# Performance work log

Measured on AMD Instinct MI355X. Metric: run time of the kernel, lower is better.

Reference implementation:

```python
import jax, jax.numpy as jnp
import numpy as np

B, L, H, M, V = 8, 1024, 1024, 128, 32
LN_EPS = 1e-5


def setup_inputs() -> dict:
    key = jax.random.key(0)
    ks = jax.random.split(key, 6)
    x_enc = jax.random.normal(ks[0], (B, L, H), dtype=jnp.float32)
    ln_gamma = jnp.ones((H,), jnp.float32)
    ln_beta = jnp.zeros((H,), jnp.float32)
    Wq = jax.random.normal(ks[1], (H, H), jnp.float32) * 0.02
    Wk = jax.random.normal(ks[2], (H, H), jnp.float32) * 0.02
    W_embed = jax.random.normal(ks[3], (V * V, H), jnp.float32) * 0.02
    W_mlm = jax.random.normal(ks[4], (V, H), jnp.float32) * 0.02
    # masked positions per sequence: contiguous span [1, M] (token 0 at pos 0,
    # token 2 at pos M+1 in the original encoding); sorted, in-range, static M.
    mask_idx = jnp.tile(jnp.arange(1, M + 1, dtype=jnp.int32)[None, :], (B, 1))
    return {"x_enc": x_enc, "ln_gamma": ln_gamma, "ln_beta": ln_beta,
            "Wq": Wq, "Wk": Wk, "W_embed": W_embed, "W_mlm": W_mlm,
            "mask_idx": mask_idx}


def _layer_norm(x, gamma, beta):
    mu = jnp.mean(x, axis=-1, keepdims=True)
    var = jnp.mean(jnp.square(x - mu), axis=-1, keepdims=True)
    return (x - mu) * jax.lax.rsqrt(var + LN_EPS) * gamma + beta


def reference(x_enc, ln_gamma, ln_beta, Wq, Wk, W_embed, W_mlm, mask_idx):
    x = _layer_norm(x_enc, ln_gamma, ln_beta)            # [B,L,H]
    mlm_logits = jnp.einsum('blh,vh->blv', x, W_mlm)      # [B,L,V]

    # ragged masked-span gather (static M masked positions per sequence)
    masked_x = jnp.take_along_axis(x, mask_idx[:, :, None].astype(jnp.int32), axis=1)  # [B,M,H]
    q = jnp.einsum('bmh,oh->bmo', masked_x, Wq)           # fc_pmlm_q, no bias
    k = jnp.einsum('bmh,oh->bmo', masked_x, Wk)           # fc_pmlm_k, no bias
    pairs = jnp.einsum('bih,bjh->bijh', q, k)             # per-span outer product [B,M,M,H]
    pairs = pairs.reshape(B * M * M, H)
    logits = jnp.einsum('nh,vh->nv', pairs, W_embed)      # [B*M*M, V*V]

    diag_mask = jnp.tile(jnp.eye(M, dtype=bool).reshape(-1), B)  # [B*M*M]

    in_span = jnp.zeros((B, L), jnp.int8).at[jnp.arange(B)[:, None], mask_idx].set(1)
    mask_aa = in_span[:, :, None]                                      # [B,L,1]
    pair_mask_aa = (in_span[:, :, None] * in_span[:, None, :])[..., None]  # [B,L,L,1] int8

    return logits, mlm_logits, diag_mask, mask_aa, pair_mask_aa
```

## Files before the change

kernel.cpp:

```cpp
#include <hip/hip_runtime.h>


typedef float   f32x4 __attribute__((ext_vector_type(4)));
typedef _Float16 f16x8 __attribute__((ext_vector_type(8)));

__device__ __forceinline__ void gld16(const void* g, void* l) {
  __builtin_amdgcn_global_load_lds(
      (const __attribute__((address_space(1))) void*)g,
      (__attribute__((address_space(3))) void*)l, 16, 0, 0);
}

__global__ __launch_bounds__(256) void cvt_kernel(
    const float* __restrict__ wq, const float* __restrict__ wk,
    const float* __restrict__ we, const float* __restrict__ wm,
    _Float16* __restrict__ oq, _Float16* __restrict__ ok,
    _Float16* __restrict__ oe, _Float16* __restrict__ om) {
  int id = blockIdx.x * 256 + threadIdx.x;
  const float* src; _Float16* dst; int off;
  if (id < 262144)      { src = wq; dst = oq; off = id; }
  else if (id < 524288) { src = wk; dst = ok; off = id - 262144; }
  else if (id < 786432) { src = we; dst = oe; off = id - 524288; }
  else                  { src = wm; dst = om; off = id - 786432; }
  float4 v = ((const float4*)src)[off];
  union { _Float16 h[4]; uint2 u; } o;
  o.h[0] = (_Float16)v.x; o.h[1] = (_Float16)v.y;
  o.h[2] = (_Float16)v.z; o.h[3] = (_Float16)v.w;
  ((uint2*)dst)[off] = o.u;
}

__global__ __launch_bounds__(256) void ln_kernel(
    const float* __restrict__ x, const float* __restrict__ g,
    const float* __restrict__ be, _Float16* __restrict__ xo) {
  const int row = blockIdx.x, t = threadIdx.x;
  const float4 v = ((const float4*)(x + (size_t)row * 1024))[t];
  float s1 = v.x + v.y + v.z + v.w;
  float s2 = v.x * v.x + v.y * v.y + v.z * v.z + v.w * v.w;
  #pragma unroll
  for (int m = 1; m < 64; m <<= 1) {
    s1 += __shfl_xor(s1, m, 64);
    s2 += __shfl_xor(s2, m, 64);
  }
  __shared__ float red[8];
  const int w = t >> 6, lane = t & 63;
  if (lane == 0) { red[w * 2] = s1; red[w * 2 + 1] = s2; }
  __syncthreads();
  s1 = red[0] + red[2] + red[4] + red[6];
  s2 = red[1] + red[3] + red[5] + red[7];
  const float mu = s1 * (1.f / 1024.f);
  const float var = s2 * (1.f / 1024.f) - mu * mu;
  const float rs = rsqrtf(var + 1e-5f);
  const float4 gv = ((const float4*)g)[t];
  const float4 bv = ((const float4*)be)[t];
  union { _Float16 h[4]; uint2 u; } o;
  o.h[0] = (_Float16)((v.x - mu) * rs * gv.x + bv.x);
  o.h[1] = (_Float16)((v.y - mu) * rs * gv.y + bv.y);
  o.h[2] = (_Float16)((v.z - mu) * rs * gv.z + bv.z);
  o.h[3] = (_Float16)((v.w - mu) * rs * gv.w + bv.w);
  ((uint2*)(xo + (size_t)row * 1024))[t] = o.u;
}

__global__ __launch_bounds__(256, 4) void qk_gemm(
    const _Float16* __restrict__ xh, const _Float16* __restrict__ wq,
    const _Float16* __restrict__ wk, const int* __restrict__ midx,
    _Float16* __restrict__ qout, _Float16* __restrict__ kout) {
  __shared__ _Float16 at[64 * 32];
  __shared__ _Float16 bt[64 * 32];
  const int tid = threadIdx.x, w = tid >> 6, lane = tid & 63;
  const int l15 = lane & 15, quad = lane >> 4;
  const int ntile = blockIdx.x, rtile = blockIdx.y, mat = blockIdx.z;
  const _Float16* wmat = mat ? wk : wq;
  _Float16* outp = mat ? kout : qout;

  const int arow = tid >> 2;
  const int acol = (tid & 3) * 8;
  const int grow = rtile * 64 + arow;
  const int b = grow >> 7, m = grow & 127;
  const int src = midx[b * 128 + m];
  const _Float16* agp = xh + ((size_t)(b * 1024 + src)) * 1024 + acol;
  const _Float16* bgp = wmat + (size_t)(ntile * 64 + arow) * 1024 + acol;
  char* aldst = (char*)at + w * 1024;
  char* bldst = (char*)bt + w * 1024;

  f32x4 acc[4];
  const f32x4 zero = {0.f, 0.f, 0.f, 0.f};
  #pragma unroll
  for (int ns = 0; ns < 4; ++ns) acc[ns] = zero;

  for (int s = 0; s < 32; ++s) {
    const int kk = s * 32;
    gld16(agp + kk, aldst);
    gld16(bgp + kk, bldst);
    __syncthreads();
    const f16x8 af = *(const f16x8*)&at[(w * 16 + l15) * 32 + quad * 8];
    #pragma unroll
    for (int ns = 0; ns < 4; ++ns) {
      const f16x8 bf = *(const f16x8*)&bt[(ns * 16 + l15) * 32 + quad * 8];
      acc[ns] = __builtin_amdgcn_mfma_f32_16x16x32_f16(af, bf, acc[ns], 0, 0, 0);
    }
    __syncthreads();
  }
  #pragma unroll
  for (int ns = 0; ns < 4; ++ns) {
    const int col = ntile * 64 + ns * 16 + l15;
    #pragma unroll
    for (int r = 0; r < 4; ++r) {
      const int row = rtile * 64 + w * 16 + quad * 4 + r;
      outp[(size_t)row * 1024 + col] = (_Float16)acc[ns][r];
    }
  }
}

__global__ __launch_bounds__(256, 3) void big_gemm(
    const _Float16* __restrict__ qf, const _Float16* __restrict__ kf,
    const _Float16* __restrict__ wemb, float* __restrict__ out) {
  __shared__ _Float16 kt[128 * 32];
  __shared__ _Float16 btile[128 * 32];
  __shared__ _Float16 qrow[1024];

  const int tid = threadIdx.x, w = tid >> 6, lane = tid & 63;
  const int l15 = lane & 15, quad = lane >> 4;
  const int vtile = blockIdx.x;
  const int rt = blockIdx.y;
  const int b = rt >> 7, i = rt & 127;
  const int wm = w >> 1, wn = w & 1;

  const _Float16* kbase = kf + (size_t)b * 128 * 1024;
  const _Float16* qbase = qf + (size_t)(b * 128 + i) * 1024;
  const _Float16* wbase = wemb + (size_t)vtile * 128 * 1024;

  if (w < 2) gld16(qbase + w * 512 + lane * 8, (char*)qrow + w * 1024);

  f32x4 acc[4][4];
  const f32x4 zero = {0.f, 0.f, 0.f, 0.f};
  #pragma unroll
  for (int a = 0; a < 4; ++a)
    #pragma unroll
    for (int c = 0; c < 4; ++c) acc[a][c] = zero;

  const int srow0 = w * 32 + (lane >> 2);
  const int scol = (lane & 3) * 8;

  for (int s = 0; s < 32; ++s) {
    const int kk = s * 32;
    #pragma unroll
    for (int p = 0; p < 2; ++p) {
      const int r = srow0 + p * 16;
      gld16(kbase + (size_t)r * 1024 + kk + scol,
            (char*)kt + w * 2048 + p * 1024);
      gld16(wbase + (size_t)r * 1024 + kk + scol,
            (char*)btile + w * 2048 + p * 1024);
    }
    __syncthreads();

    const f16x8 qs = *(const f16x8*)&qrow[kk + quad * 8];
    f16x8 af[4], bf[4];
    #pragma unroll
    for (int ms = 0; ms < 4; ++ms) {
      const f16x8 kfr = *(const f16x8*)&kt[(wm * 64 + ms * 16 + l15) * 32 + quad * 8];
      af[ms] = kfr * qs;
    }
    #pragma unroll
    for (int ns = 0; ns < 4; ++ns)
      bf[ns] = *(const f16x8*)&btile[(wn * 64 + ns * 16 + l15) * 32 + quad * 8];
    #pragma unroll
    for (int ms = 0; ms < 4; ++ms)
      #pragma unroll
      for (int ns = 0; ns < 4; ++ns)
        acc[ms][ns] = __builtin_amdgcn_mfma_f32_16x16x32_f16(af[ms], bf[ns],
                                                             acc[ms][ns], 0, 0, 0);
    __syncthreads();
  }

  const size_t nbase = (size_t)rt * 128;
  #pragma unroll
  for (int ms = 0; ms < 4; ++ms) {
    const int j0 = wm * 64 + ms * 16 + quad * 4;
    #pragma unroll
    for (int ns = 0; ns < 4; ++ns) {
      const int col = vtile * 128 + wn * 64 + ns * 16 + l15;
      #pragma unroll
      for (int r = 0; r < 4; ++r)
        out[(nbase + j0 + r) * 1024 + col] = acc[ms][ns][r];
    }
  }
}

__global__ __launch_bounds__(256) void mlm_kernel(
    const _Float16* __restrict__ xh, const _Float16* __restrict__ wm,
    float* __restrict__ out) {
  const int w = threadIdx.x >> 6, lane = threadIdx.x & 63;
  const int row = blockIdx.x * 4 + w;
  const int v = lane & 31, part = lane >> 5;
  const f16x8* xr = (const f16x8*)(xh + (size_t)row * 1024 + part * 512);
  const f16x8* wr = (const f16x8*)(wm + (size_t)v * 1024 + part * 512);
  float acc = 0.f;
  #pragma unroll 8
  for (int it = 0; it < 64; ++it) {
    const f16x8 p = xr[it] * wr[it];
    #pragma unroll
    for (int e = 0; e < 8; ++e) acc += (float)p[e];
  }
  acc += __shfl_xor(acc, 32, 64);
  if (part == 0) out[(size_t)row * 32 + v] = acc;
}

__global__ __launch_bounds__(256) void span_kernel(
    const int* __restrict__ midx, float* __restrict__ mask_aa,
    float* __restrict__ diag, float* __restrict__ span_ws) {
  __shared__ float flag[1024];
  const int b = blockIdx.x, t = threadIdx.x;
  for (int p = t; p < 1024; p += 256) flag[p] = 0.f;
  __syncthreads();
  if (t < 128) flag[midx[b * 128 + t]] = 1.f;
  __syncthreads();
  for (int p = t; p < 1024; p += 256) {
    const float f = flag[p];
    mask_aa[b * 1024 + p] = f;
    span_ws[b * 1024 + p] = f;
  }
  for (int p = t; p < 16384; p += 256)
    diag[b * 16384 + p] = ((p >> 7) == (p & 127)) ? 1.f : 0.f;
}

__global__ __launch_bounds__(256) void pairmask_kernel(
    const float* __restrict__ span_ws, float* __restrict__ out) {
  const int id = blockIdx.x * 256 + threadIdx.x;
  const int b = id >> 18;
  const int rem = id & 262143;
  const int i = rem >> 8;
  const int j4 = rem & 255;
  const float si = span_ws[b * 1024 + i];
  const float4 sj = ((const float4*)(span_ws + b * 1024))[j4];
  float4 o;
  o.x = si * sj.x; o.y = si * sj.y; o.z = si * sj.z; o.w = si * sj.w;
  ((float4*)out)[id] = o;
}

extern "C" void kernel_launch(void* const* d_in, const int* in_sizes, int n_in,
                              void* d_out, int out_size, void* d_ws, size_t ws_size,
                              hipStream_t stream) {
  const float* x_enc = (const float*)d_in[0];
  const float* gam   = (const float*)d_in[1];
  const float* bet   = (const float*)d_in[2];
  const float* Wq    = (const float*)d_in[3];
  const float* Wk    = (const float*)d_in[4];
  const float* We    = (const float*)d_in[5];
  const float* Wm    = (const float*)d_in[6];
  const int*   midx  = (const int*)d_in[7];
  float* out = (float*)d_out;

  char* ws = (char*)d_ws;
  _Float16* x_h  = (_Float16*)(ws);
  _Float16* q_h  = (_Float16*)(ws + ((size_t)16 << 20));
  _Float16* k_h  = (_Float16*)(ws + ((size_t)18 << 20));
  _Float16* wq_h = (_Float16*)(ws + ((size_t)20 << 20));
  _Float16* wk_h = (_Float16*)(ws + ((size_t)22 << 20));
  _Float16* we_h = (_Float16*)(ws + ((size_t)24 << 20));
  _Float16* wm_h = (_Float16*)(ws + ((size_t)26 << 20));
  float* span_ws = (float*)(ws + ((size_t)27 << 20));

  float* o_logits = out;
  float* o_mlm    = out + (size_t)134217728;
  float* o_diag   = o_mlm + 262144;
  float* o_maskaa = o_diag + 131072;
  float* o_pair   = o_maskaa + 8192;

  cvt_kernel<<<3104, 256, 0, stream>>>(Wq, Wk, We, Wm, wq_h, wk_h, we_h, wm_h);
  ln_kernel<<<8192, 256, 0, stream>>>(x_enc, gam, bet, x_h);
  qk_gemm<<<dim3(16, 16, 2), 256, 0, stream>>>(x_h, wq_h, wk_h, midx, q_h, k_h);
  big_gemm<<<dim3(8, 1024), 256, 0, stream>>>(q_h, k_h, we_h, o_logits);
  mlm_kernel<<<2048, 256, 0, stream>>>(x_h, wm_h, o_mlm);
  span_kernel<<<8, 256, 0, stream>>>(midx, o_maskaa, o_diag, span_ws);
  pairmask_kernel<<<8192, 256, 0, stream>>>(span_ws, o_pair);
}
```

Before: 925.8 us.

## Restructure pair-logits GEMM into 256x256 tiles with triple-buffered swizzled LDS pipeline

```diff
diff --git a/kernel.cpp b/kernel.cpp
--- a/kernel.cpp
+++ b/kernel.cpp
@@ -110,79 +110,150 @@
   }
 }
 
-__global__ __launch_bounds__(256, 3) void big_gemm(
+#define BG_BUF 49152
+#define BG_WE  16384
+#define BG_Q   147456
+__global__ __launch_bounds__(512, 2) void big_gemm(
     const _Float16* __restrict__ qf, const _Float16* __restrict__ kf,
     const _Float16* __restrict__ wemb, float* __restrict__ out) {
-  __shared__ _Float16 kt[128 * 32];
-  __shared__ _Float16 btile[128 * 32];
-  __shared__ _Float16 qrow[1024];
-
-  const int tid = threadIdx.x, w = tid >> 6, lane = tid & 63;
+  __shared__ __align__(16) char lds[151552];
+  const int tid = threadIdx.x;
+  const int w = tid >> 6, lane = tid & 63;
   const int l15 = lane & 15, quad = lane >> 4;
-  const int vtile = blockIdx.x;
-  const int rt = blockIdx.y;
-  const int b = rt >> 7, i = rt & 127;
-  const int wm = w >> 1, wn = w & 1;
-
-  const _Float16* kbase = kf + (size_t)b * 128 * 1024;
-  const _Float16* qbase = qf + (size_t)(b * 128 + i) * 1024;
-  const _Float16* wbase = wemb + (size_t)vtile * 128 * 1024;
-
-  if (w < 2) gld16(qbase + w * 512 + lane * 8, (char*)qrow + w * 1024);
-
-  f32x4 acc[4][4];
-  const f32x4 zero = {0.f, 0.f, 0.f, 0.f};
-  #pragma unroll
-  for (int a = 0; a < 4; ++a)
-    #pragma unroll
-    for (int c = 0; c < 4; ++c) acc[a][c] = zero;
-
-  const int srow0 = w * 32 + (lane >> 2);
-  const int scol = (lane & 3) * 8;
-
-  for (int s = 0; s < 32; ++s) {
-    const int kk = s * 32;
-    #pragma unroll
-    for (int p = 0; p < 2; ++p) {
-      const int r = srow0 + p * 16;
-      gld16(kbase + (size_t)r * 1024 + kk + scol,
-            (char*)kt + w * 2048 + p * 1024);
-      gld16(wbase + (size_t)r * 1024 + kk + scol,
-            (char*)btile + w * 2048 + p * 1024);
-    }
-    __syncthreads();
-
-    const f16x8 qs = *(const f16x8*)&qrow[kk + quad * 8];
-    f16x8 af[4], bf[4];
-    #pragma unroll
-    for (int ms = 0; ms < 4; ++ms) {
-      const f16x8 kfr = *(const f16x8*)&kt[(wm * 64 + ms * 16 + l15) * 32 + quad * 8];
-      af[ms] = kfr * qs;
-    }
-    #pragma unroll
-    for (int ns = 0; ns < 4; ++ns)
-      bf[ns] = *(const f16x8*)&btile[(wn * 64 + ns * 16 + l15) * 32 + quad * 8];
-    #pragma unroll
-    for (int ms = 0; ms < 4; ++ms)
-      #pragma unroll
-      for (int ns = 0; ns < 4; ++ns)
-        acc[ms][ns] = __builtin_amdgcn_mfma_f32_16x16x32_f16(af[ms], bf[ns],
-                                                             acc[ms][ns], 0, 0, 0);
-    __syncthreads();
-  }
-
-  const size_t nbase = (size_t)rt * 128;
-  #pragma unroll
-  for (int ms = 0; ms < 4; ++ms) {
-    const int j0 = wm * 64 + ms * 16 + quad * 4;
+  const int wm = w >> 2, wn = w & 3;
+  const int rtile = blockIdx.x;
+  const int vtile = blockIdx.y;
+  const int b = rtile >> 6;
+  const int i0 = (rtile & 63) * 2;
+
+  const int lrow = lane >> 3;
+  const int cgsw = (lane & 7) ^ lrow;
+  const char* kg = (const char*)(kf + (size_t)b * 128 * 1024);
+  const char* wg = (const char*)(wemb + (size_t)vtile * 256 * 1024);
+  const char* ks0 = kg + (size_t)(((w)      * 8 + lrow) * 2048 + cgsw * 16);
+  const char* ks1 = kg + (size_t)(((w + 8)  * 8 + lrow) * 2048 + cgsw * 16);
+  const char* ws0 = wg + (size_t)(((w)      * 8 + lrow) * 2048 + cgsw * 16);
+  const char* ws1 = wg + (size_t)(((w + 8)  * 8 + lrow) * 2048 + cgsw * 16);
+  const char* ws2 = wg + (size_t)(((w + 16) * 8 + lrow) * 2048 + cgsw * 16);
+  const char* ws3 = wg + (size_t)(((w + 24) * 8 + lrow) * 2048 + cgsw * 16);
+  const int kd0 = w * 1024,          kd1 = (w + 8) * 1024;
+  const int wd0 = BG_WE + w * 1024,  wd1 = BG_WE + (w + 8) * 1024;
+  const int wd2 = BG_WE + (w + 16) * 1024, wd3 = BG_WE + (w + 24) * 1024;
+
+  const int swzb = (l15 & 7) << 4;
+  const int col0 = (quad * 16) ^ swzb;
+  const int col1 = (64 + quad * 16) ^ swzb;
+  const int abase = l15 * 128;
+  const int bbase = BG_WE + (wn * 64 + l15) * 128;
+  const int qbase = BG_Q + wm * 2048 + quad * 16;
+
+  if (w < 4) {
+    const char* qsrc = (const char*)(qf + (size_t)(b * 128 + i0 + (w >> 1)) * 1024)
+                       + (w & 1) * 1024 + lane * 16;
+    gld16(qsrc, lds + BG_Q + w * 1024);
+  }
+  gld16(ks0, lds + kd0);              gld16(ks1, lds + kd1);
+  gld16(ws0, lds + wd0);              gld16(ws1, lds + wd1);
+  gld16(ws2, lds + wd2);              gld16(ws3, lds + wd3);
+  gld16(ks0 + 128, lds + BG_BUF + kd0); gld16(ks1 + 128, lds + BG_BUF + kd1);
+  gld16(ws0 + 128, lds + BG_BUF + wd0); gld16(ws1 + 128, lds + BG_BUF + wd1);
+  gld16(ws2 + 128, lds + BG_BUF + wd2); gld16(ws3 + 128, lds + BG_BUF + wd3);
+
+  f32x4 acc[8][4];
+  #pragma unroll
+  for (int a = 0; a < 8; ++a)
+    #pragma unroll
+    for (int c = 0; c < 4; ++c) acc[a][c] = (f32x4){0.f, 0.f, 0.f, 0.f};
+
+  f16x8 af[4][2], bf0[2][2], bf1[2][2], qs0, qs1;
+
+#define RD_A(mh)                                                               \
+  _Pragma("unroll")                                                            \
+  for (int ms = 0; ms < 4; ++ms) {                                             \
+    af[ms][0] = *(const f16x8*)(lds + cb + abase + (mh) * 8192 + ms * 2048 + col0); \
+    af[ms][1] = *(const f16x8*)(lds + cb + abase + (mh) * 8192 + ms * 2048 + col1); \
+  }
+#define RD_B(dst, nh)                                                          \
+  _Pragma("unroll")                                                            \
+  for (int ns = 0; ns < 2; ++ns) {                                             \
+    dst[ns][0] = *(const f16x8*)(lds + cb + bbase + (nh) * 4096 + ns * 2048 + col0); \
+    dst[ns][1] = *(const f16x8*)(lds + cb + bbase + (nh) * 4096 + ns * 2048 + col1); \
+  }
+#define MULT_A()                                                               \
+  _Pragma("unroll")                                                            \
+  for (int ms = 0; ms < 4; ++ms) { af[ms][0] *= qs0; af[ms][1] *= qs1; }
+#define MFMA8(MH, NH, BFR)                                                     \
+  __builtin_amdgcn_s_setprio(1);                                               \
+  _Pragma("unroll")                                                            \
+  for (int kh = 0; kh < 2; ++kh)                                               \
+    _Pragma("unroll")                                                          \
+    for (int ms = 0; ms < 4; ++ms)                                             \
+      _Pragma("unroll")                                                        \
+      for (int ns = 0; ns < 2; ++ns)                                           \
+        acc[(MH) * 4 + ms][(NH) * 2 + ns] = __builtin_amdgcn_mfma_f32_16x16x32_f16( \
+            af[ms][kh], BFR[ns][kh], acc[(MH) * 4 + ms][(NH) * 2 + ns], 0, 0, 0);   \
+  __builtin_amdgcn_s_setprio(0);
+#define BAR() __builtin_amdgcn_s_barrier()
+#define LGKM0() asm volatile("s_waitcnt lgkmcnt(0)" ::: "memory")
+
+  int cur = 0;
+  #pragma unroll 1
+  for (int t = 0; t < 16; ++t) {
+    const int cb = cur * BG_BUF;
+    int stg = cur + 2; if (stg >= 3) stg -= 3;
+    const int sb = stg * BG_BUF;
+    const int skb = (t + 2) * 128;
+    const bool st = (t < 14);
+
+    if (t < 15) asm volatile("s_waitcnt vmcnt(6)" ::: "memory");
+    else        asm volatile("s_waitcnt vmcnt(0)" ::: "memory");
+    BAR();
+
+    qs0 = *(const f16x8*)(lds + qbase + t * 128);
+    qs1 = *(const f16x8*)(lds + qbase + t * 128 + 64);
+    RD_A(0)
+    RD_B(bf0, 0)
+    if (st) { gld16(ks0 + skb, lds + sb + kd0); gld16(ks1 + skb, lds + sb + kd1); }
+    BAR(); LGKM0();
+    MULT_A()
+    MFMA8(0, 0, bf0)
+    BAR();
+    RD_B(bf1, 1)
+    if (st) { gld16(ws0 + skb, lds + sb + wd0); gld16(ws1 + skb, lds + sb + wd1); }
+    BAR(); LGKM0();
+    MFMA8(0, 1, bf1)
+    BAR();
+    RD_A(1)
+    if (st) { gld16(ws2 + skb, lds + sb + wd2); gld16(ws3 + skb, lds + sb + wd3); }
+    BAR(); LGKM0();
+    MULT_A()
+    MFMA8(1, 1, bf1)
+    BAR();
+    BAR(); LGKM0();
+    MFMA8(1, 0, bf0)
+    BAR();
+
+    cur = cur + 1; if (cur == 3) cur = 0;
+  }
+
+  const size_t nb = (size_t)((b * 128 + i0 + wm)) * 128;
+  const int colb = vtile * 256 + wn * 64;
+  #pragma unroll
+  for (int ms = 0; ms < 8; ++ms) {
     #pragma unroll
     for (int ns = 0; ns < 4; ++ns) {
-      const int col = vtile * 128 + wn * 64 + ns * 16 + l15;
       #pragma unroll
       for (int r = 0; r < 4; ++r)
-        out[(nbase + j0 + r) * 1024 + col] = acc[ms][ns][r];
+        out[(nb + ms * 16 + quad * 4 + r) * 1024 + colb + ns * 16 + l15] =
+            acc[ms][ns][r];
     }
   }
+#undef RD_A
+#undef RD_B
+#undef MULT_A
+#undef MFMA8
+#undef BAR
+#undef LGKM0
 }
 
 __global__ __launch_bounds__(256) void mlm_kernel(
@@ -268,7 +339,7 @@
   cvt_kernel<<<3104, 256, 0, stream>>>(Wq, Wk, We, Wm, wq_h, wk_h, we_h, wm_h);
   ln_kernel<<<8192, 256, 0, stream>>>(x_enc, gam, bet, x_h);
   qk_gemm<<<dim3(16, 16, 2), 256, 0, stream>>>(x_h, wq_h, wk_h, midx, q_h, k_h);
-  big_gemm<<<dim3(8, 1024), 256, 0, stream>>>(q_h, k_h, we_h, o_logits);
+  big_gemm<<<dim3(512, 4), 512, 0, stream>>>(q_h, k_h, we_h, o_logits);
   mlm_kernel<<<2048, 256, 0, stream>>>(x_h, wm_h, o_mlm);
   span_kernel<<<8, 256, 0, stream>>>(midx, o_maskaa, o_diag, span_ws);
   pairmask_kernel<<<8192, 256, 0, stream>>>(span_ws, o_pair);
```

Result: faster. 904.3 us (-2.3%).
